# Kernel optimization log

Measured on AMD Instinct MI355X. Metric: run time of the kernel, lower is better.

The kernel has to match this reference:

```python
import jax, jax.numpy as jnp
import numpy as np

RAY_START, RAY_END = 2.25, 3.3
DEPTH_RES, N_IMPORTANCE = 48, 48
BOX_WARP = 1.0
PLANE_AXES = jnp.array([[[1.,0.,0.],[0.,1.,0.],[0.,0.,1.]],
                        [[1.,0.,0.],[0.,0.,1.],[0.,1.,0.]],
                        [[0.,0.,1.],[1.,0.,0.],[0.,1.,0.]]], jnp.float32)


def grid_sample_bilinear(feat, gx, gy):
    # feat [B,C,H,W]; gx,gy [B,M] in [-1,1]; bilinear, zeros padding, align_corners=False
    B, C, H, W = feat.shape
    x = (gx + 1.0) * (W * 0.5) - 0.5
    y = (gy + 1.0) * (H * 0.5) - 0.5
    x0 = jnp.floor(x); y0 = jnp.floor(y)
    wx = (x - x0)[:, None, :]; wy = (y - y0)[:, None, :]
    x0i = x0.astype(jnp.int32); y0i = y0.astype(jnp.int32)
    flat = feat.reshape(B, C, H * W)
    def gather(xi, yi):
        valid = ((xi >= 0) & (xi < W) & (yi >= 0) & (yi < H)).astype(feat.dtype)
        idx = jnp.clip(yi, 0, H - 1) * W + jnp.clip(xi, 0, W - 1)
        v = jnp.take_along_axis(flat, jnp.broadcast_to(idx[:, None, :], (B, C, idx.shape[-1])), axis=2)
        return v * valid[:, None, :]
    v00 = gather(x0i, y0i); v10 = gather(x0i + 1, y0i)
    v01 = gather(x0i, y0i + 1); v11 = gather(x0i + 1, y0i + 1)
    return (v00 * (1 - wx) * (1 - wy) + v10 * wx * (1 - wy)
            + v01 * (1 - wx) * wy + v11 * wx * wy)  # [B,C,M]


def sample_from_planes(planes_feat, coords):
    # planes_feat [N,3,C,H,W], coords [N,M,3] -> [N,3,M,C]
    N, P, C, H, W = planes_feat.shape
    M = coords.shape[1]
    c = (2.0 / BOX_WARP) * coords
    inv = jnp.linalg.inv(PLANE_AXES)  # [P,3,3]
    proj = jnp.einsum('nmi,pij->npmj', c, inv)[..., :2]
    out = grid_sample_bilinear(planes_feat.reshape(N * P, C, H, W),
                               proj[..., 0].reshape(N * P, M),
                               proj[..., 1].reshape(N * P, M))
    return out.reshape(N, P, C, M).transpose(0, 1, 3, 2)


def decode(feats, w1, b1, w2, b2):
    # OSGDecoder: mean over planes, Linear->softplus->Linear
    x = feats.mean(axis=1)
    h = jax.nn.softplus(x @ w1 + b1)
    o = h @ w2 + b2
    sigma = o[..., :1]
    rgb = jax.nn.sigmoid(o[..., 1:]) * (1 + 2 * 0.001) - 0.001
    return rgb, sigma


def ray_march(colors, densities, depths, color_bg=None):
    # MipRayMarcher2 with softplus density clamp and BG compositing via final transmittance
    deltas = depths[:, :, 1:] - depths[:, :, :-1]
    colors_mid = 0.5 * (colors[:, :, :-1] + colors[:, :, 1:])
    densities_mid = jax.nn.softplus(0.5 * (densities[:, :, :-1] + densities[:, :, 1:]) - 1.0)
    depths_mid = 0.5 * (depths[:, :, :-1] + depths[:, :, 1:])
    alpha = 1.0 - jnp.exp(-densities_mid * deltas)
    alpha_shifted = jnp.concatenate([jnp.ones_like(alpha[:, :, :1]), 1 - alpha + 1e-10], axis=2)
    T = jnp.cumprod(alpha_shifted, axis=2)
    weights = alpha * T[:, :, :-1]
    comp_rgb = (weights * colors_mid).sum(axis=2)
    weight_total = weights.sum(axis=2)
    comp_depth = jnp.nan_to_num((weights * depths_mid).sum(axis=2) / weight_total, nan=float('inf'))
    comp_depth = jnp.clip(comp_depth, depths.min(), depths.max())
    bg_trans = T[:, :, -1]  # [B,R,1]
    if color_bg is not None:
        comp_rgb = comp_rgb + bg_trans * color_bg
    comp_rgb = comp_rgb * 2.0 - 1.0
    return comp_rgb, comp_depth, weights, alpha, bg_trans


def sample_pdf(bins, weights, n_importance, eps=1e-5):
    # inverse-CDF importance sampling (deterministic midpoint u)
    nw = weights.shape[-1]
    weights = weights + eps
    pdf = weights / weights.sum(axis=-1, keepdims=True)
    cdf = jnp.concatenate([jnp.zeros_like(pdf[:, :1]), jnp.cumsum(pdf, axis=-1)], axis=-1)
    u = (jnp.arange(n_importance, dtype=cdf.dtype) + 0.5) / n_importance
    u = jnp.broadcast_to(u, (cdf.shape[0], n_importance))
    inds = jax.vmap(lambda c, uu: jnp.searchsorted(c, uu, side='right'))(cdf, u)
    below = jnp.clip(inds - 1, 0, nw)
    above = jnp.clip(inds, 0, nw)
    cdf_b = jnp.take_along_axis(cdf, below, axis=-1)
    cdf_a = jnp.take_along_axis(cdf, above, axis=-1)
    bins_b = jnp.take_along_axis(bins, below, axis=-1)
    bins_a = jnp.take_along_axis(bins, above, axis=-1)
    denom = jnp.where(cdf_a - cdf_b < eps, 1.0, cdf_a - cdf_b)
    return bins_b + (u - cdf_b) / denom * (bins_a - bins_b)


def sample_importance(z_vals, weights, n_importance):
    B, R, S, _ = z_vals.shape
    z = z_vals.reshape(B * R, S)
    w = weights.reshape(B * R, -1) + 0.01
    wp = jnp.pad(w, ((0, 0), (1, 1)), constant_values=-np.inf)
    w = jnp.maximum(wp[:, :-1], wp[:, 1:])      # max_pool1d(k=2,s=1,p=1)
    w = 0.5 * (w[:, :-1] + w[:, 1:]) + 0.01     # avg_pool1d(k=2,s=1)
    z_mid = 0.5 * (z[:, :-1] + z[:, 1:])
    z_fine = sample_pdf(z_mid, w[:, 1:-1], n_importance)
    return jax.lax.stop_gradient(z_fine).reshape(B, R, n_importance, 1)


def unify_samples(d1, c1, s1, d2, c2, s2):
    depths = jnp.concatenate([d1, d2], axis=2)
    colors = jnp.concatenate([c1, c2], axis=2)
    dens = jnp.concatenate([s1, s2], axis=2)
    idx = jnp.argsort(depths, axis=2)
    depths = jnp.take_along_axis(depths, idx, axis=2)
    colors = jnp.take_along_axis(colors, jnp.broadcast_to(idx, colors.shape), axis=2)
    dens = jnp.take_along_axis(dens, idx, axis=2)
    return depths, colors, dens


def sample_stratified(B, R, dtype):
    S = DEPTH_RES
    delta = (RAY_END - RAY_START) / (S - 1)
    d = jnp.linspace(RAY_START, RAY_END, S, dtype=dtype).reshape(1, 1, S, 1) + 0.5 * delta
    return jnp.broadcast_to(d, (B, R, S, 1))


def setup_inputs() -> dict:
    key = jax.random.key(0)
    ks = jax.random.split(key, 10)
    B, R, C, H = 4, 4096, 32, 256
    planes = 0.1 * jax.random.normal(ks[0], (B, 3, C, H, H), jnp.float32)
    ray_origins = jnp.array([0.0, 0.0, 2.7]) + 0.03 * jax.random.normal(ks[1], (B, R, 3), jnp.float32)
    uv = jax.random.uniform(ks[2], (B, R, 2), jnp.float32, -0.4, 0.4)
    d = jnp.concatenate([uv, -jnp.ones((B, R, 1), jnp.float32)], axis=-1)
    ray_directions = d / jnp.linalg.norm(d, axis=-1, keepdims=True)
    z_bg = jax.random.normal(ks[3], (B, 64), jnp.float32)
    dec_w1 = jax.random.normal(ks[4], (C, 64), jnp.float32) / np.sqrt(C)
    dec_b1 = jnp.zeros((64,), jnp.float32)
    dec_w2 = jax.random.normal(ks[5], (64, 33), jnp.float32) / 8.0
    dec_b2 = jnp.zeros((33,), jnp.float32)
    bg_w1 = jax.random.normal(ks[6], (67, 64), jnp.float32) / np.sqrt(67)
    bg_b1 = jnp.zeros((64,), jnp.float32)
    bg_w2 = jax.random.normal(ks[7], (64, 32), jnp.float32) / 8.0
    bg_b2 = jnp.zeros((32,), jnp.float32)
    return dict(planes=planes, ray_origins=ray_origins, ray_directions=ray_directions, z_bg=z_bg,
                dec_w1=dec_w1, dec_b1=dec_b1, dec_w2=dec_w2, dec_b2=dec_b2,
                bg_w1=bg_w1, bg_b1=bg_b1, bg_w2=bg_w2, bg_b2=bg_b2)


def reference(planes, ray_origins, ray_directions, z_bg, dec_w1, dec_b1, dec_w2, dec_b2,
              bg_w1, bg_b1, bg_w2, bg_b2):
    B, R, _ = ray_origins.shape
    S = DEPTH_RES
    depths_coarse = sample_stratified(B, R, planes.dtype)
    coords = (ray_origins[:, :, None, :] + depths_coarse * ray_directions[:, :, None, :]).reshape(B, -1, 3)
    feats = sample_from_planes(planes, coords)
    rgb_c, sig_c = decode(feats, dec_w1, dec_b1, dec_w2, dec_b2)
    rgb_c = rgb_c.reshape(B, R, S, -1)
    sig_c = sig_c.reshape(B, R, S, 1)
    # Ball background feature: MLP on [dir, z_bg]
    z = jnp.broadcast_to(z_bg[:, None, :], (B, R, z_bg.shape[-1]))
    hb = jax.nn.softplus(jnp.concatenate([ray_directions, z], axis=-1) @ bg_w1 + bg_b1)
    color_bg = jax.nn.sigmoid(hb @ bg_w2 + bg_b2)  # [B,R,32]
    _, _, w_coarse, _, _ = ray_march(rgb_c, sig_c, depths_coarse)
    depths_fine = sample_importance(depths_coarse, w_coarse, N_IMPORTANCE)
    coords_f = (ray_origins[:, :, None, :] + depths_fine * ray_directions[:, :, None, :]).reshape(B, -1, 3)
    feats_f = sample_from_planes(planes, coords_f)
    rgb_f, sig_f = decode(feats_f, dec_w1, dec_b1, dec_w2, dec_b2)
    rgb_f = rgb_f.reshape(B, R, N_IMPORTANCE, -1)
    sig_f = sig_f.reshape(B, R, N_IMPORTANCE, 1)
    depths_all, rgb_all, sig_all = unify_samples(depths_coarse, rgb_c, sig_c, depths_fine, rgb_f, sig_f)
    rgb_final, depth_final, weights, alpha, bg_T = ray_march(rgb_all, sig_all, depths_all, color_bg)
    return rgb_final, depth_final, weights.sum(axis=2)
```

## Files before the change

kernel.cpp:

```cpp
#include <hip/hip_runtime.h>
#include <hip/hip_bf16.h>
#include <math.h>

#define NB 4
#define NR 4096
#define NC 32
#define NH 256
#define NW 256
#define NS 48
#define NRAYS (NB*NR)
#define NSAMP (NRAYS*NS)

__device__ __forceinline__ float coarse_depth(int i) {
    const float DELTA = 1.05f / 47.f;
    return 2.25f + i * DELTA + 0.5f * DELTA;
}
__device__ __forceinline__ float zmid_c(int i) {
    return 0.5f * (coarse_depth(i) + coarse_depth(i + 1));
}
__device__ __forceinline__ float softplus_f(float x) {
    return fmaxf(x, 0.f) + __logf(1.f + __expf(-fabsf(x)));
}
__device__ __forceinline__ float sigmoid_f(float x) {
    return __frcp_rn(1.f + __expf(-x));
}

__global__ __launch_bounds__(256) void k_transpose(const float* __restrict__ in,
                                                   float* __restrict__ out) {
    __shared__ float tile[32][65];
    int bp = blockIdx.x >> 10;
    int t0 = (blockIdx.x & 1023) * 64;
    const float* src = in + (size_t)bp * NC * NH * NW;
    float* dst = out + (size_t)bp * NH * NW * NC;
    int px = threadIdx.x & 63;
    int c0 = threadIdx.x >> 6;
    #pragma unroll
    for (int cc = 0; cc < 32; cc += 4)
        tile[cc + c0][px] = src[(size_t)(cc + c0) * NH * NW + t0 + px];
    __syncthreads();
    int c = threadIdx.x & 31;
    int p0 = threadIdx.x >> 5;
    #pragma unroll
    for (int pp = 0; pp < 64; pp += 8)
        dst[(size_t)(t0 + pp + p0) * NC + c] = tile[c][pp + p0];
}

__global__ __launch_bounds__(256) void k_prep(const float* __restrict__ w1,
                                              const float* __restrict__ w2,
                                              float* __restrict__ w1t,
                                              float* __restrict__ w2p) {
    for (int i = threadIdx.x; i < 2048; i += 256) {
        int j = i >> 5, c = i & 31;
        w1t[j * 32 + c] = w1[c * 64 + j];
    }
    for (int i = threadIdx.x; i < 64 * 36; i += 256) {
        int j = i / 36, kx = i - j * 36;
        w2p[i] = (kx < 33) ? w2[j * 33 + kx] : 0.f;
    }
}

template<bool FINE>
__global__ __launch_bounds__(256) void k_gather(
    const float* __restrict__ planes_t,
    const float* __restrict__ origins,
    const float* __restrict__ dirs,
    const float* __restrict__ dfine,
    float* __restrict__ feats_out)
{
    int lane  = threadIdx.x & 63;
    int wbase = threadIdx.x & 192;
    int s0    = blockIdx.x * 256 + wbase;

    int s   = s0 + lane;
    int ray = s / NS;
    int kk  = s - ray * NS;
    float t = FINE ? dfine[s] : coarse_depth(kk);
    float ox = origins[ray*3+0], oy = origins[ray*3+1], oz = origins[ray*3+2];
    float ddx = dirs[ray*3+0],   ddy = dirs[ray*3+1],   ddz = dirs[ray*3+2];
    float cx = 2.f * (ox + t * ddx);
    float cy = 2.f * (oy + t * ddy);
    float cz = 2.f * (oz + t * ddz);
    int bi = ray >> 12;
    int   m_base[3];
    float m_q[3][4];
    #pragma unroll
    for (int p = 0; p < 3; ++p) {
        float gx = (p == 2) ? cz : cx;
        float gy = (p == 0) ? cy : ((p == 1) ? cz : cx);
        float fx = (gx + 1.f) * 128.f - 0.5f;
        float fy = (gy + 1.f) * 128.f - 0.5f;
        float x0f = floorf(fx), y0f = floorf(fy);
        float wx = fx - x0f, wy = fy - y0f;
        int x0 = (int)x0f, y0 = (int)y0f;
        if (x0 >= -1 && x0 <= 255 && y0 >= -1 && y0 <= 255) {
            float wxm = 1.f - wx, wym = 1.f - wy;
            float q00 = wxm*wym, q10 = wx*wym, q01 = wxm*wy, q11 = wx*wy;
            if (!(x0 >= 0   && y0 >= 0))   q00 = 0.f;
            if (!(x0 <= 254 && y0 >= 0))   q10 = 0.f;
            if (!(x0 >= 0   && y0 <= 254)) q01 = 0.f;
            if (!(x0 <= 254 && y0 <= 254)) q11 = 0.f;
            m_base[p] = (bi*3 + p) * (NH*NW*NC) + (y0*NW + x0)*NC;
            m_q[p][0] = q00; m_q[p][1] = q10; m_q[p][2] = q01; m_q[p][3] = q11;
        } else {
            m_base[p] = -1;
            m_q[p][0] = m_q[p][1] = m_q[p][2] = m_q[p][3] = 0.f;
        }
    }

    int ch   = lane & 31;
    int half = lane >> 5;
    #pragma unroll 1
    for (int i = 0; i < 64; i += 2) {
        int src = i + half;
        float acc = 0.f;
        #pragma unroll
        for (int p = 0; p < 3; ++p) {
            int   bse = __shfl(m_base[p], src);
            float q00 = __shfl(m_q[p][0], src);
            float q10 = __shfl(m_q[p][1], src);
            float q01 = __shfl(m_q[p][2], src);
            float q11 = __shfl(m_q[p][3], src);
            if (bse >= 0) {
                const float* ptr = planes_t + (size_t)bse + ch;
                acc += q00 * ptr[0]    + q10 * ptr[32]
                     + q01 * ptr[8192] + q11 * ptr[8224];
            }
        }
        feats_out[(size_t)(s0 + i + half) * 32 + ch] = acc * (1.f / 3.f);
    }
}

__global__ __launch_bounds__(256, 4) void k_mlp(
    const float* __restrict__ w1t,
    const float* __restrict__ b1,
    const float* __restrict__ w2p,
    const float* __restrict__ b2,
    float* __restrict__ rgb_io,
    float* __restrict__ sig_out)
{
    int s = blockIdx.x * 256 + threadIdx.x;
    float* base = rgb_io + (size_t)s * 32;
    float x[32];
    #pragma unroll
    for (int i = 0; i < 8; ++i) {
        float4 v = ((const float4*)base)[i];
        x[4*i+0] = v.x; x[4*i+1] = v.y; x[4*i+2] = v.z; x[4*i+3] = v.w;
    }
    float o[33];
    #pragma unroll
    for (int k2 = 0; k2 < 33; ++k2) o[k2] = b2[k2];
    #pragma unroll 4
    for (int j = 0; j < 64; ++j) {
        float a = b1[j];
        #pragma unroll
        for (int c = 0; c < 32; ++c) a += x[c] * w1t[j * 32 + c];
        float h = softplus_f(a);
        #pragma unroll
        for (int k2 = 0; k2 < 33; ++k2) o[k2] += h * w2p[j * 36 + k2];
    }
    sig_out[s] = o[0];
    #pragma unroll
    for (int i = 0; i < 8; ++i) {
        float4 r;
        r.x = sigmoid_f(o[1 + 4*i + 0]) * 1.002f - 0.001f;
        r.y = sigmoid_f(o[1 + 4*i + 1]) * 1.002f - 0.001f;
        r.z = sigmoid_f(o[1 + 4*i + 2]) * 1.002f - 0.001f;
        r.w = sigmoid_f(o[1 + 4*i + 3]) * 1.002f - 0.001f;
        ((float4*)base)[i] = r;
    }
}

__global__ __launch_bounds__(256) void k_importance(const float* __restrict__ sig,
                                                    float* __restrict__ dfine) {
    int ray = blockIdx.x * 256 + threadIdx.x;
    const float* sp = sig + (size_t)ray * NS;
    float w[47];
    float T = 1.f;
    float sprev = sp[0];
    #pragma unroll
    for (int i = 0; i < 47; ++i) {
        float scur = sp[i + 1];
        float dens = softplus_f(0.5f * (sprev + scur) - 1.f);
        float delta = coarse_depth(i + 1) - coarse_depth(i);
        float alpha = 1.f - __expf(-dens * delta);
        w[i] = alpha * T + 0.01f;
        T *= (1.f - alpha + 1e-10f);
        sprev = scur;
    }
    float p[45];
    float sum = 0.f;
    #pragma unroll
    for (int i = 1; i <= 45; ++i) {
        float nwi  = fmaxf(w[i - 1], w[i]);
        float nwi1 = fmaxf(w[i], w[i + 1]);
        float wb = 0.5f * (nwi + nwi1) + 0.01f;
        float v = wb + 1e-5f;
        p[i - 1] = v;
        sum += v;
    }
    int k = 0;
    float cdf_lo = 0.f;
    #pragma unroll
    for (int i = 0; i < 45; ++i) {
        float cdf_hi = cdf_lo + p[i] / sum;
        float bb = zmid_c(i), ba = zmid_c(i + 1);
        float denom = cdf_hi - cdf_lo;
        if (denom < 1e-5f) denom = 1.f;
        while (k < 48) {
            float u = (k + 0.5f) / 48.f;
            if (u < cdf_hi) {
                dfine[(size_t)ray * NS + k] = bb + (u - cdf_lo) / denom * (ba - bb);
                ++k;
            } else break;
        }
        cdf_lo = cdf_hi;
    }
    while (k < 48) {
        dfine[(size_t)ray * NS + k] = zmid_c(45);
        ++k;
    }
}

__global__ __launch_bounds__(256) void k_final(
    const float* __restrict__ sig_c, const float* __restrict__ rgb_c,
    const float* __restrict__ sig_f, const float* __restrict__ rgb_f,
    const float* __restrict__ dfine,
    const float* __restrict__ dirs, const float* __restrict__ z_bg,
    const float* __restrict__ bw1, const float* __restrict__ bb1,
    const float* __restrict__ bw2, const float* __restrict__ bb2,
    float* __restrict__ out_rgb, float* __restrict__ out_dep,
    float* __restrict__ out_wt)
{
    __shared__ float s_d[4][96];
    __shared__ float s_sig[4][96];
    __shared__ int   s_src[4][96];
    __shared__ float s_fine[4][48];
    __shared__ float s_w[4][96];
    __shared__ float s_g[4][96];
    __shared__ float s_h[4][64];
    __shared__ float s_zb[64];
    int lane = threadIdx.x & 63;
    int wv = threadIdx.x >> 6;
    int ray = blockIdx.x * 4 + wv;
    int bi = (blockIdx.x * 4) >> 12;
    if (threadIdx.x < 64) s_zb[threadIdx.x] = z_bg[bi * 64 + threadIdx.x];
    if (lane < 48) s_fine[wv][lane] = dfine[(size_t)ray * NS + lane];
    __syncthreads();

    if (lane < 48) {
        float cd = coarse_depth(lane);
        int lo = 0, hi = 48;
        while (lo < hi) { int mid = (lo + hi) >> 1;
            if (s_fine[wv][mid] < cd) lo = mid + 1; else hi = mid; }
        int rc = lane + lo;
        s_d[wv][rc] = cd;
        s_sig[wv][rc] = sig_c[(size_t)ray * NS + lane];
        s_src[wv][rc] = lane;
        float f = s_fine[wv][lane];
        lo = 0; hi = 48;
        while (lo < hi) { int mid = (lo + hi) >> 1;
            if (coarse_depth(mid) <= f) lo = mid + 1; else hi = mid; }
        int rf = lane + lo;
        s_d[wv][rf] = f;
        s_sig[wv][rf] = sig_f[(size_t)ray * NS + lane];
        s_src[wv][rf] = 48 + lane;
    }
    float ddx = dirs[ray*3+0], ddy = dirs[ray*3+1], ddz = dirs[ray*3+2];
    __syncthreads();

    float alpha0 = 0.f, alpha1 = 0.f, a0 = 1.f, a1 = 1.f;
    float dm0 = 0.f, dm1 = 0.f;
    if (lane < 48) {
        int i0 = 2 * lane, i1 = i0 + 1;
        float d0 = s_d[wv][i0], sA = s_sig[wv][i0];
        float d1 = s_d[wv][i1], sB = s_sig[wv][i1];
        {
            float dens = softplus_f(0.5f * (sA + sB) - 1.f);
            alpha0 = 1.f - __expf(-dens * (d1 - d0));
            a0 = 1.f - alpha0 + 1e-10f;
            dm0 = 0.5f * (d0 + d1);
        }
        if (i1 < 95) {
            float d2 = s_d[wv][i1 + 1], sC = s_sig[wv][i1 + 1];
            float dens = softplus_f(0.5f * (sB + sC) - 1.f);
            alpha1 = 1.f - __expf(-dens * (d2 - d1));
            a1 = 1.f - alpha1 + 1e-10f;
            dm1 = 0.5f * (d1 + d2);
        }
    }
    float P = a0 * a1;
    #pragma unroll
    for (int off = 1; off < 64; off <<= 1) {
        float t = __shfl_up(P, off);
        if (lane >= off) P *= t;
    }
    float T_all = __shfl(P, 63);
    float E = __shfl_up(P, 1);
    if (lane == 0) E = 1.f;
    float w0 = alpha0 * E;
    float w1 = alpha1 * (E * a0);
    float sw = w0 + w1;
    float sd = w0 * dm0 + w1 * dm1;
    #pragma unroll
    for (int off = 32; off; off >>= 1) {
        sw += __shfl_xor(sw, off);
        sd += __shfl_xor(sd, off);
    }
    if (lane < 48) {
        s_w[wv][2 * lane] = w0;
        s_w[wv][2 * lane + 1] = w1;
    }
    __syncthreads();
    {
        int i = lane;
        float wm = (i > 0) ? s_w[wv][i - 1] : 0.f;
        s_g[wv][i] = 0.5f * (wm + s_w[wv][i]);
        int i2 = lane + 64;
        if (lane < 32)
            s_g[wv][i2] = 0.5f * (s_w[wv][i2 - 1] + s_w[wv][i2]);
    }

    float a = bb1[lane] + ddx * bw1[lane] + ddy * bw1[64 + lane] + ddz * bw1[128 + lane];
    #pragma unroll 1
    for (int i = 0; i < 64; ++i) a += s_zb[i] * bw1[(3 + i) * 64 + lane];
    s_h[wv][lane] = softplus_f(a);
    __syncthreads();
    int c = lane & 31;
    float ob = bb2[c];
    #pragma unroll 1
    for (int j = 0; j < 64; ++j) ob += s_h[wv][j] * bw2[j * 32 + c];
    float bgc = sigmoid_f(ob);

    int h = lane >> 5;
    size_t rbase = (size_t)ray * NS * 32;
    const float* b0p = rgb_c + rbase;
    const float* b1p = rgb_f + rbase - (size_t)48 * 32;
    float acc = 0.f;
    #pragma unroll 4
    for (int i = h; i < 96; i += 2) {
        int src = s_src[wv][i];
        const float* cp = ((src < 48) ? b0p : b1p) + (size_t)src * 32;
        acc += s_g[wv][i] * cp[c];
    }
    acc += __shfl_xor(acc, 32);

    float rgbv = (acc + T_all * bgc) * 2.f - 1.f;
    float dep = sd / sw;
    if (!(dep == dep)) dep = INFINITY;
    dep = fminf(fmaxf(dep, coarse_depth(0)), coarse_depth(47));
    if (lane < 32) out_rgb[(size_t)ray * 32 + c] = rgbv;
    if (lane == 0) { out_dep[ray] = dep; out_wt[ray] = sw; }
}

extern "C" void kernel_launch(void* const* d_in, const int* in_sizes, int n_in,
                              void* d_out, int out_size, void* d_ws, size_t ws_size,
                              hipStream_t stream) {
    (void)in_sizes; (void)n_in; (void)out_size; (void)ws_size;
    const float* planes  = (const float*)d_in[0];
    const float* origins = (const float*)d_in[1];
    const float* dirs    = (const float*)d_in[2];
    const float* z_bg    = (const float*)d_in[3];
    const float* dw1     = (const float*)d_in[4];
    const float* db1     = (const float*)d_in[5];
    const float* dw2     = (const float*)d_in[6];
    const float* db2     = (const float*)d_in[7];
    const float* bw1     = (const float*)d_in[8];
    const float* bb1     = (const float*)d_in[9];
    const float* bw2     = (const float*)d_in[10];
    const float* bb2     = (const float*)d_in[11];

    char* ws = (char*)d_ws;
    size_t off = 0;
    float* sig_c    = (float*)(ws + off); off += (size_t)NSAMP * 4;
    float* sig_f    = (float*)(ws + off); off += (size_t)NSAMP * 4;
    float* dfine    = (float*)(ws + off); off += (size_t)NSAMP * 4;
    float* w1t      = (float*)(ws + off); off += 64 * 32 * 4;
    float* w2p      = (float*)(ws + off); off += 64 * 36 * 4;
    float* planes_t = (float*)(ws + off); off += (size_t)NB * 3 * NH * NW * NC * 4;
    float* rgb_c    = (float*)(ws + off); off += (size_t)NSAMP * 32 * 4;
    float* rgb_f    = (float*)(ws + off); off += (size_t)NSAMP * 32 * 4;

    float* out_rgb = (float*)d_out;
    float* out_dep = out_rgb + (size_t)NRAYS * 32;
    float* out_wt  = out_dep + NRAYS;

    k_prep<<<dim3(1), dim3(256), 0, stream>>>(dw1, dw2, w1t, w2p);
    k_transpose<<<dim3(NB * 3 * 1024), dim3(256), 0, stream>>>(planes, planes_t);
    k_gather<false><<<dim3(NSAMP / 256), dim3(256), 0, stream>>>(
        planes_t, origins, dirs, (const float*)nullptr, rgb_c);
    k_mlp<<<dim3(NSAMP / 256), dim3(256), 0, stream>>>(
        w1t, db1, w2p, db2, rgb_c, sig_c);
    k_importance<<<dim3(NRAYS / 256), dim3(256), 0, stream>>>(sig_c, dfine);
    k_gather<true><<<dim3(NSAMP / 256), dim3(256), 0, stream>>>(
        planes_t, origins, dirs, dfine, rgb_f);
    k_mlp<<<dim3(NSAMP / 256), dim3(256), 0, stream>>>(
        w1t, db1, w2p, db2, rgb_f, sig_f);
    k_final<<<dim3(NRAYS / 4), dim3(256), 0, stream>>>(
        sig_c, rgb_c, sig_f, rgb_f, dfine, dirs, z_bg,
        bw1, bb1, bw2, bb2, out_rgb, out_dep, out_wt);
}
```

Baseline: 770.7 us.

## Split fine-pass MLP across four threads per sample with shared hidden buffer

```diff
diff --git a/kernel.cpp b/kernel.cpp
--- a/kernel.cpp
+++ b/kernel.cpp
@@ -47,8 +47,11 @@
 
 __global__ __launch_bounds__(256) void k_prep(const float* __restrict__ w1,
                                               const float* __restrict__ w2,
+                                              const float* __restrict__ b2,
                                               float* __restrict__ w1t,
-                                              float* __restrict__ w2p) {
+                                              float* __restrict__ w2p,
+                                              float* __restrict__ w2q,
+                                              float* __restrict__ bq) {
     for (int i = threadIdx.x; i < 2048; i += 256) {
         int j = i >> 5, c = i & 31;
         w1t[j * 32 + c] = w1[c * 64 + j];
@@ -56,6 +59,21 @@
     for (int i = threadIdx.x; i < 64 * 36; i += 256) {
         int j = i / 36, kx = i - j * 36;
         w2p[i] = (kx < 33) ? w2[j * 33 + kx] : 0.f;
+    }
+    for (int i = threadIdx.x; i < 64 * 48; i += 256) {
+        int j = i / 48, r = i - j * 48;
+        int q = r / 12, kk = r - q * 12;
+        int col; bool valid;
+        if (q == 0) { col = kk;            valid = kk < 9; }
+        else        { col = 8 * q + kk + 1; valid = kk < 8; }
+        w2q[i] = valid ? w2[j * 33 + col] : 0.f;
+    }
+    if (threadIdx.x < 48) {
+        int q = threadIdx.x / 12, kk = threadIdx.x - q * 12;
+        int col; bool valid;
+        if (q == 0) { col = kk;            valid = kk < 9; }
+        else        { col = 8 * q + kk + 1; valid = kk < 8; }
+        bq[threadIdx.x] = valid ? b2[col] : 0.f;
     }
 }
 
@@ -130,7 +148,9 @@
     }
 }
 
-__global__ __launch_bounds__(256, 4) void k_mlp(
+__global__ __launch_bounds__(256)
+__attribute__((amdgpu_waves_per_eu(3, 5)))
+void k_mlp(
     const float* __restrict__ w1t,
     const float* __restrict__ b1,
     const float* __restrict__ w2p,
@@ -168,6 +188,65 @@
         r.w = sigmoid_f(o[1 + 4*i + 3]) * 1.002f - 0.001f;
         ((float4*)base)[i] = r;
     }
+}
+
+__global__ __launch_bounds__(256)
+__attribute__((amdgpu_waves_per_eu(4, 7)))
+void k_mlp2(
+    const float* __restrict__ w1t,
+    const float* __restrict__ b1,
+    const float* __restrict__ w2q,
+    const float* __restrict__ bq,
+    float* __restrict__ rgb_io,
+    float* __restrict__ sig_out)
+{
+    __shared__ float hs[64 * 68];
+    int q  = threadIdx.x & 3;
+    int sl = threadIdx.x >> 2;
+    int s  = blockIdx.x * 64 + sl;
+    const float* xp = rgb_io + (size_t)s * 32;
+    float x[32];
+    #pragma unroll
+    for (int i = 0; i < 8; ++i) {
+        float4 v = ((const float4*)xp)[i];
+        x[4*i+0] = v.x; x[4*i+1] = v.y; x[4*i+2] = v.z; x[4*i+3] = v.w;
+    }
+    int j0 = q * 16;
+    float h[16];
+    #pragma unroll
+    for (int jj = 0; jj < 16; ++jj) {
+        int j = j0 + jj;
+        float a = b1[j];
+        #pragma unroll
+        for (int c = 0; c < 32; ++c) a += x[c] * w1t[j * 32 + c];
+        h[jj] = softplus_f(a);
+    }
+    float* hrow = hs + sl * 68 + j0;
+    #pragma unroll
+    for (int i = 0; i < 4; ++i)
+        ((float4*)hrow)[i] = make_float4(h[4*i], h[4*i+1], h[4*i+2], h[4*i+3]);
+
+    float o[9];
+    #pragma unroll
+    for (int kk = 0; kk < 9; ++kk) o[kk] = bq[q * 12 + kk];
+    const float* hbase = hs + sl * 68;
+    #pragma unroll 4
+    for (int j = 0; j < 64; ++j) {
+        float hj = hbase[j];
+        const float* wr = w2q + j * 48 + q * 12;
+        #pragma unroll
+        for (int kk = 0; kk < 9; ++kk) o[kk] += hj * wr[kk];
+    }
+    if (q == 0) sig_out[s] = o[0];
+    float r[8];
+    #pragma unroll
+    for (int i = 0; i < 8; ++i) {
+        float ov = (q == 0) ? o[i + 1] : o[i];
+        r[i] = sigmoid_f(ov) * 1.002f - 0.001f;
+    }
+    float* outp = rgb_io + (size_t)s * 32 + q * 8;
+    ((float4*)outp)[0] = make_float4(r[0], r[1], r[2], r[3]);
+    ((float4*)outp)[1] = make_float4(r[4], r[5], r[6], r[7]);
 }
 
 __global__ __launch_bounds__(256) void k_importance(const float* __restrict__ sig,
@@ -376,6 +455,8 @@
     float* dfine    = (float*)(ws + off); off += (size_t)NSAMP * 4;
     float* w1t      = (float*)(ws + off); off += 64 * 32 * 4;
     float* w2p      = (float*)(ws + off); off += 64 * 36 * 4;
+    float* w2q      = (float*)(ws + off); off += 64 * 48 * 4;
+    float* bq       = (float*)(ws + off); off += 256;
     float* planes_t = (float*)(ws + off); off += (size_t)NB * 3 * NH * NW * NC * 4;
     float* rgb_c    = (float*)(ws + off); off += (size_t)NSAMP * 32 * 4;
     float* rgb_f    = (float*)(ws + off); off += (size_t)NSAMP * 32 * 4;
@@ -384,7 +465,7 @@
     float* out_dep = out_rgb + (size_t)NRAYS * 32;
     float* out_wt  = out_dep + NRAYS;
 
-    k_prep<<<dim3(1), dim3(256), 0, stream>>>(dw1, dw2, w1t, w2p);
+    k_prep<<<dim3(1), dim3(256), 0, stream>>>(dw1, dw2, db2, w1t, w2p, w2q, bq);
     k_transpose<<<dim3(NB * 3 * 1024), dim3(256), 0, stream>>>(planes, planes_t);
     k_gather<false><<<dim3(NSAMP / 256), dim3(256), 0, stream>>>(
         planes_t, origins, dirs, (const float*)nullptr, rgb_c);
@@ -393,8 +474,8 @@
     k_importance<<<dim3(NRAYS / 256), dim3(256), 0, stream>>>(sig_c, dfine);
     k_gather<true><<<dim3(NSAMP / 256), dim3(256), 0, stream>>>(
         planes_t, origins, dirs, dfine, rgb_f);
-    k_mlp<<<dim3(NSAMP / 256), dim3(256), 0, stream>>>(
-        w1t, db1, w2p, db2, rgb_f, sig_f);
+    k_mlp2<<<dim3(NSAMP / 64), dim3(256), 0, stream>>>(
+        w1t, db1, w2q, bq, rgb_f, sig_f);
     k_final<<<dim3(NRAYS / 4), dim3(256), 0, stream>>>(
         sig_c, rgb_c, sig_f, rgb_f, dfine, dirs, z_bg,
         bw1, bb1, bw2, bb2, out_rgb, out_dep, out_wt);
```

Result: slower. 1.608 ms (+108.7%).

## Split coarse MLP across thread pairs with shuffle-reduced hidden layer

Applied to the files above, without the earlier changes.

```diff
diff --git a/kernel.cpp b/kernel.cpp
--- a/kernel.cpp
+++ b/kernel.cpp
@@ -47,8 +47,11 @@
 
 __global__ __launch_bounds__(256) void k_prep(const float* __restrict__ w1,
                                               const float* __restrict__ w2,
+                                              const float* __restrict__ b2,
                                               float* __restrict__ w1t,
-                                              float* __restrict__ w2p) {
+                                              float* __restrict__ w2p,
+                                              float* __restrict__ w2s,
+                                              float* __restrict__ bq2) {
     for (int i = threadIdx.x; i < 2048; i += 256) {
         int j = i >> 5, c = i & 31;
         w1t[j * 32 + c] = w1[c * 64 + j];
@@ -56,6 +59,21 @@
     for (int i = threadIdx.x; i < 64 * 36; i += 256) {
         int j = i / 36, kx = i - j * 36;
         w2p[i] = (kx < 33) ? w2[j * 33 + kx] : 0.f;
+    }
+    for (int i = threadIdx.x; i < 64 * 40; i += 256) {
+        int j = i / 40, r = i - j * 40;
+        int e = r / 20, k = r - e * 20;
+        float v = 0.f;
+        if (e == 0) { if (k < 17) v = w2[j * 33 + k]; }
+        else        { if (k >= 1 && k < 17) v = w2[j * 33 + 16 + k]; }
+        w2s[i] = v;
+    }
+    if (threadIdx.x < 40) {
+        int e = threadIdx.x / 20, k = threadIdx.x - e * 20;
+        float v = 0.f;
+        if (e == 0) { if (k < 17) v = b2[k]; }
+        else        { if (k >= 1 && k < 17) v = b2[16 + k]; }
+        bq2[threadIdx.x] = v;
     }
 }
 
@@ -130,7 +148,9 @@
     }
 }
 
-__global__ __launch_bounds__(256, 4) void k_mlp(
+__global__ __launch_bounds__(256)
+__attribute__((amdgpu_waves_per_eu(3, 5)))
+void k_mlp(
     const float* __restrict__ w1t,
     const float* __restrict__ b1,
     const float* __restrict__ w2p,
@@ -167,6 +187,52 @@
         r.z = sigmoid_f(o[1 + 4*i + 2]) * 1.002f - 0.001f;
         r.w = sigmoid_f(o[1 + 4*i + 3]) * 1.002f - 0.001f;
         ((float4*)base)[i] = r;
+    }
+}
+
+__global__ __launch_bounds__(256) void k_mlp_pair(
+    const float* __restrict__ w1t,
+    const float* __restrict__ b1,
+    const float* __restrict__ w2s,
+    const float* __restrict__ bq2,
+    float* __restrict__ rgb_io,
+    float* __restrict__ sig_out)
+{
+    int t = blockIdx.x * 256 + threadIdx.x;
+    int s = t >> 1;
+    int e = t & 1;
+    float* xp = rgb_io + (size_t)s * 32 + e * 16;
+    float x[16];
+    #pragma unroll
+    for (int i = 0; i < 4; ++i) {
+        float4 v = ((const float4*)xp)[i];
+        x[4*i+0] = v.x; x[4*i+1] = v.y; x[4*i+2] = v.z; x[4*i+3] = v.w;
+    }
+    const float* bb = bq2 + e * 20;
+    float o[17];
+    #pragma unroll
+    for (int k = 0; k < 17; ++k) o[k] = bb[k];
+    const float* w1base = w1t + e * 16;
+    const float* w2base = w2s + e * 20;
+    #pragma unroll 4
+    for (int j = 0; j < 64; ++j) {
+        float a = 0.f;
+        #pragma unroll
+        for (int c = 0; c < 16; ++c) a += x[c] * w1base[j * 32 + c];
+        a += __shfl_xor(a, 1);
+        float h = softplus_f(a + b1[j]);
+        #pragma unroll
+        for (int k = 0; k < 17; ++k) o[k] += h * w2base[j * 40 + k];
+    }
+    if (e == 0) sig_out[s] = o[0];
+    #pragma unroll
+    for (int i = 0; i < 4; ++i) {
+        float4 r;
+        r.x = sigmoid_f(o[1 + 4*i + 0]) * 1.002f - 0.001f;
+        r.y = sigmoid_f(o[1 + 4*i + 1]) * 1.002f - 0.001f;
+        r.z = sigmoid_f(o[1 + 4*i + 2]) * 1.002f - 0.001f;
+        r.w = sigmoid_f(o[1 + 4*i + 3]) * 1.002f - 0.001f;
+        ((float4*)xp)[i] = r;
     }
 }
 
@@ -376,6 +442,8 @@
     float* dfine    = (float*)(ws + off); off += (size_t)NSAMP * 4;
     float* w1t      = (float*)(ws + off); off += 64 * 32 * 4;
     float* w2p      = (float*)(ws + off); off += 64 * 36 * 4;
+    float* w2s      = (float*)(ws + off); off += 64 * 40 * 4;
+    float* bq2      = (float*)(ws + off); off += 256;
     float* planes_t = (float*)(ws + off); off += (size_t)NB * 3 * NH * NW * NC * 4;
     float* rgb_c    = (float*)(ws + off); off += (size_t)NSAMP * 32 * 4;
     float* rgb_f    = (float*)(ws + off); off += (size_t)NSAMP * 32 * 4;
@@ -384,12 +452,12 @@
     float* out_dep = out_rgb + (size_t)NRAYS * 32;
     float* out_wt  = out_dep + NRAYS;
 
-    k_prep<<<dim3(1), dim3(256), 0, stream>>>(dw1, dw2, w1t, w2p);
+    k_prep<<<dim3(1), dim3(256), 0, stream>>>(dw1, dw2, db2, w1t, w2p, w2s, bq2);
     k_transpose<<<dim3(NB * 3 * 1024), dim3(256), 0, stream>>>(planes, planes_t);
     k_gather<false><<<dim3(NSAMP / 256), dim3(256), 0, stream>>>(
         planes_t, origins, dirs, (const float*)nullptr, rgb_c);
-    k_mlp<<<dim3(NSAMP / 256), dim3(256), 0, stream>>>(
-        w1t, db1, w2p, db2, rgb_c, sig_c);
+    k_mlp_pair<<<dim3(NSAMP * 2 / 256), dim3(256), 0, stream>>>(
+        w1t, db1, w2s, bq2, rgb_c, sig_c);
     k_importance<<<dim3(NRAYS / 256), dim3(256), 0, stream>>>(sig_c, dfine);
     k_gather<true><<<dim3(NSAMP / 256), dim3(256), 0, stream>>>(
         planes_t, origins, dirs, dfine, rgb_f);
```

New measurement: 1.038 ms. +34.7%, slower.
